# Optimization experiments

Hardware: AMD Instinct MI355X
Metric: run time of the kernel (lower is better)

## Reference

```python
import jax, jax.numpy as jnp
import numpy as np

N_COARSE = 12500
N_FINE = 50000
MIN_BASIS = 16  # (min(L_in, L_out) + 1) ** 2 with L_in = L_out = 3


def setup_inputs() -> dict:
    key = jax.random.key(0)
    ks = jax.random.split(key, 8)
    return {
        "last_inv": jax.random.normal(ks[0], (N_COARSE, 256), dtype=jnp.float32),
        "cur_inv": jax.random.normal(ks[1], (N_FINE, 256), dtype=jnp.float32),
        "last_equ": jax.random.normal(ks[2], (N_COARSE, 16, 256), dtype=jnp.float32),
        "cur_equ": jax.random.normal(ks[3], (N_FINE, 16, 256), dtype=jnp.float32),
        "upsampling": jax.random.randint(ks[4], (N_FINE,), 0, N_COARSE, dtype=jnp.int32),
        # Linear weights stored as [in, out] (torch weight is [out, in]; x @ W.T == x @ W_in_out)
        "W_last_equ": jax.random.normal(ks[5], (256, 256), dtype=jnp.float32) * 0.02,
        "W_cur_equ": jax.random.normal(ks[6], (256, 256), dtype=jnp.float32) * 0.02,
        "W_mlp": jax.random.normal(ks[7], (768, 512), dtype=jnp.float32) * 0.02,
    }


def reference(last_inv, cur_inv, last_equ, cur_equ, upsampling, W_last_equ, W_cur_equ, W_mlp):
    # nearest_upsample: gather coarse rows up to fine resolution
    li = jnp.take(last_inv, upsampling, axis=0)                 # [N_fine, 256]
    le = jnp.take(last_equ, upsampling, axis=0)[:, :MIN_BASIS]  # [N_fine, 16, 256]
    le = jnp.einsum('nbc,cd->nbd', le, W_last_equ)              # fc_last_equ (no bias)
    ce = jnp.einsum('nbc,cd->nbd', cur_equ[:, :MIN_BASIS], W_cur_equ)  # fc_cur_equ
    equ = (ce * le).mean(axis=1)                                # [N_fine, 256]
    com = jnp.concatenate([li, cur_inv, equ], axis=-1)          # [N_fine, 768]
    return com @ W_mlp                                          # LastUnaryBlock: Linear, no bias
```

## Files before the change

### kernel.cpp

```cpp
#include <hip/hip_runtime.h>
#include <hip/hip_bf16.h>

#define N_COARSE 12500
#define N_FINE   50000

typedef __bf16 bf16x8 __attribute__((ext_vector_type(8)));
typedef __bf16 bf16x4 __attribute__((ext_vector_type(4)));
typedef float  f32x4  __attribute__((ext_vector_type(4)));


__device__ __forceinline__ bf16x8 cvt8(f32x4 x, f32x4 y) {
    bf16x8 r;
    r[0] = (__bf16)x[0]; r[1] = (__bf16)x[1]; r[2] = (__bf16)x[2]; r[3] = (__bf16)x[3];
    r[4] = (__bf16)y[0]; r[5] = (__bf16)y[1]; r[6] = (__bf16)y[2]; r[7] = (__bf16)y[3];
    return r;
}

__device__ __forceinline__ void lds_barrier() {
    asm volatile("s_waitcnt lgkmcnt(0)" ::: "memory");
    __builtin_amdgcn_s_barrier();
}

__device__ __forceinline__ void gl_lds16(const float* g, float* l) {
    __builtin_amdgcn_global_load_lds(
        (const __attribute__((address_space(1))) void*)g,
        (__attribute__((address_space(3))) void*)l, 16, 0, 0);
}

__device__ __forceinline__ int swz(int row, int byte) { return byte ^ ((row & 7) << 4); }
__device__ __forceinline__ void st_a(__bf16* lds, int row, int cs, bf16x8 v) {
    *(bf16x8*)((char*)lds + swz(row, row * 512 + cs * 16)) = v;
}
__device__ __forceinline__ bf16x8 ld_a(const __bf16* lds, int row, int ka) {
    return *(const bf16x8*)((const char*)lds + swz(row, row * 512 + ka * 2));
}

template<int NT>
__device__ __forceinline__ void stage_f32(const float* __restrict__ A, long row0,
                                          __bf16* lds, int tid, long maxrow) {
    const int r0 = tid >> 5, cs = tid & 31;
    constexpr int RPI = NT / 32;
    #pragma unroll
    for (int i = 0; i < 64 / RPI; ++i) {
        int row = r0 + i * RPI;
        long gr = row0 + row; if (gr > maxrow) gr = maxrow;
        const float* p = A + gr * 256 + cs * 8;
        f32x4 x = *(const f32x4*)p, y = *(const f32x4*)(p + 4);
        st_a(lds, row, cs, cvt8(x, y));
    }
}

__device__ __forceinline__ void mfma_tile(const __bf16* lds, const bf16x8* __restrict__ packB,
                                          int N, int c0, int ksb,
                                          f32x4 (&acc)[4][4], int lane) {
    const int g = lane >> 4, r15 = lane & 15;
    #pragma unroll
    for (int ks = 0; ks < 8; ++ks) {
        bf16x8 a[4];
        #pragma unroll
        for (int rt = 0; rt < 4; ++rt)
            a[rt] = ld_a(lds, rt * 16 + r15, ks * 32 + g * 8);
        const size_t kb = (size_t)((ksb + ks) * 4 + g) * N;
        #pragma unroll
        for (int ct = 0; ct < 4; ++ct) {
            bf16x8 b = packB[kb + c0 + ct * 16 + r15];
            #pragma unroll
            for (int rt = 0; rt < 4; ++rt)
                acc[rt][ct] = __builtin_amdgcn_mfma_f32_16x16x32_bf16(a[rt], b, acc[rt][ct], 0, 0, 0);
        }
    }
}

__global__ __launch_bounds__(256) void k_prep(
    const float* __restrict__ W_le, const float* __restrict__ W_ce,
    const float* __restrict__ W_mlp, const float* __restrict__ last_inv,
    __bf16* __restrict__ packLE, __bf16* __restrict__ packCE,
    __bf16* __restrict__ packM, __bf16* __restrict__ li_bf)
{
    const int b = blockIdx.x, tid = threadIdx.x;
    if (b < 256) {
        int idx = b * 256 + tid, k = idx >> 8, n = idx & 255;
        packLE[(((size_t)(k >> 3) << 8) + n) * 8 + (k & 7)] = (__bf16)W_le[idx];
    } else if (b < 512) {
        int idx = (b - 256) * 256 + tid, k = idx >> 8, n = idx & 255;
        packCE[(((size_t)(k >> 3) << 8) + n) * 8 + (k & 7)] = (__bf16)W_ce[idx];
    } else if (b < 2048) {
        int idx = (b - 512) * 256 + tid, k = idx >> 9, n = idx & 511;
        packM[(((size_t)(k >> 3) << 9) + n) * 8 + (k & 7)] = (__bf16)W_mlp[idx];
    } else {
        int i = (b - 2048) * 256 + tid;
        f32x4 v = ((const f32x4*)last_inv)[i];
        bf16x4 o;
        o[0] = (__bf16)v[0]; o[1] = (__bf16)v[1]; o[2] = (__bf16)v[2]; o[3] = (__bf16)v[3];
        ((bf16x4*)li_bf)[i] = o;
    }
}

__global__ __launch_bounds__(256) void k_coarse_equ(
    const float* __restrict__ last_equ, const bf16x8* __restrict__ packW,
    __bf16* __restrict__ LEp)
{
    __shared__ __attribute__((aligned(16))) __bf16 As[64 * 256];
    const int tid = threadIdx.x, lane = tid & 63, wid = tid >> 6;
    for (int t = blockIdx.x; t < N_COARSE * 16 / 64; t += gridDim.x) {
        stage_f32<256>(last_equ, (long)t * 64, As, tid, (long)N_COARSE * 16 - 1);
        lds_barrier();
        f32x4 acc[4][4] = {};
        mfma_tile(As, packW, 256, wid * 64, 0, acc, lane);
        #pragma unroll
        for (int rt = 0; rt < 4; ++rt) {
            int coarse = t * 4 + rt;
            #pragma unroll
            for (int ct = 0; ct < 4; ++ct) {
                int cg = wid * 4 + ct;
                bf16x4 v;
                v[0] = (__bf16)acc[rt][ct][0]; v[1] = (__bf16)acc[rt][ct][1];
                v[2] = (__bf16)acc[rt][ct][2]; v[3] = (__bf16)acc[rt][ct][3];
                *(bf16x4*)(LEp + ((size_t)(coarse * 16 + cg) * 64 + lane) * 4) = v;
            }
        }
        lds_barrier();
    }
}

__global__ __launch_bounds__(256) void k_fine_equ(
    const float* __restrict__ cur_equ, const bf16x8* __restrict__ packW,
    const __bf16* __restrict__ LEp, const int* __restrict__ up,
    __bf16* __restrict__ equ)
{
    __shared__ __attribute__((aligned(16))) float Af[2][32 * 256];
    const int tid = threadIdx.x, lane = tid & 63, wid = tid >> 6;
    const int g = lane >> 4, r15 = lane & 15;
    const int NT = N_FINE / 2;
    const int per = (NT + gridDim.x - 1) / gridDim.x;
    const int tb = blockIdx.x * per;
    const int te = min(tb + per, NT);
    if (tb >= te) return;

    const int lhalf = (lane & 1) << 2;

    {
        const float* rb = cur_equ + (size_t)tb * 32 * 256;
        #pragma unroll
        for (int i = 0; i < 8; ++i) {
            int row = wid * 8 + i;
            gl_lds16(rb + (size_t)row * 256 + ((((lane >> 1) ^ (row & 7)) << 3) + lhalf),
                     &Af[tb & 1][row * 256]);
        }
    }

    for (int t = tb; t < te; ++t) {
        asm volatile("s_waitcnt vmcnt(0)" ::: "memory");
        __builtin_amdgcn_s_barrier();

        if (t + 1 < te) {
            const float* rb = cur_equ + (size_t)(t + 1) * 32 * 256;
            #pragma unroll
            for (int i = 0; i < 8; ++i) {
                int row = wid * 8 + i;
                gl_lds16(rb + (size_t)row * 256 + ((((lane >> 1) ^ (row & 7)) << 3) + lhalf),
                         &Af[(t + 1) & 1][row * 256]);
            }
        }

        const float* B = Af[t & 1];
        f32x4 acc[2][4] = {};
        #pragma unroll
        for (int ks = 0; ks < 8; ++ks) {
            bf16x8 a[2];
            #pragma unroll
            for (int rt = 0; rt < 2; ++rt) {
                int r = rt * 16 + r15;
                const float* p = B + r * 256 + (((4 * ks + g) ^ (r & 7)) << 3);
                a[rt] = cvt8(*(const f32x4*)p, *(const f32x4*)(p + 4));
            }
            const size_t kb = (size_t)(ks * 4 + g) * 256;
            #pragma unroll
            for (int ct = 0; ct < 4; ++ct) {
                bf16x8 b = packW[kb + wid * 64 + ct * 16 + r15];
                #pragma unroll
                for (int rt = 0; rt < 2; ++rt)
                    acc[rt][ct] = __builtin_amdgcn_mfma_f32_16x16x32_bf16(a[rt], b, acc[rt][ct], 0, 0, 0);
            }
        }

        const int n0 = t * 2;
        const int cu0 = up[n0], cu1 = up[n0 + 1];
        bf16x4 le[2][4];
        #pragma unroll
        for (int ct = 0; ct < 4; ++ct) {
            le[0][ct] = *(const bf16x4*)(LEp + ((size_t)(cu0 * 16 + wid * 4 + ct) * 64 + lane) * 4);
            le[1][ct] = *(const bf16x4*)(LEp + ((size_t)(cu1 * 16 + wid * 4 + ct) * 64 + lane) * 4);
        }
        #pragma unroll
        for (int rt = 0; rt < 2; ++rt) {
            #pragma unroll
            for (int ct = 0; ct < 4; ++ct) {
                float s = acc[rt][ct][0] * (float)le[rt][ct][0]
                        + acc[rt][ct][1] * (float)le[rt][ct][1]
                        + acc[rt][ct][2] * (float)le[rt][ct][2]
                        + acc[rt][ct][3] * (float)le[rt][ct][3];
                s += __shfl_xor(s, 16, 64);
                s += __shfl_xor(s, 32, 64);
                if (lane < 16)
                    equ[(size_t)(n0 + rt) * 256 + wid * 64 + ct * 16 + lane] =
                        (__bf16)(s * 0.0625f);
            }
        }
    }
}

__global__ __launch_bounds__(512) void k_out(
    const __bf16* __restrict__ li_bf, const float* __restrict__ cur_inv,
    const __bf16* __restrict__ equ, const bf16x8* __restrict__ packW,
    const int* __restrict__ up, float* __restrict__ out)
{
    __shared__ __attribute__((aligned(16))) __bf16 As[64 * 256];
    const int tid = threadIdx.x, lane = tid & 63, wid = tid >> 6;
    const int row0 = blockIdx.x * 64;
    const int c0 = wid * 64;
    const int r0 = tid >> 5, cs = tid & 31;
    f32x4 acc[4][4] = {};

    #pragma unroll
    for (int i = 0; i < 4; ++i) {
        int row = r0 + i * 16;
        int gr = row0 + row; if (gr > N_FINE - 1) gr = N_FINE - 1;
        st_a(As, row, cs, *(const bf16x8*)(li_bf + (size_t)up[gr] * 256 + cs * 8));
    }
    lds_barrier();
    mfma_tile(As, packW, 512, c0, 0, acc, lane);
    lds_barrier();

    stage_f32<512>(cur_inv, row0, As, tid, N_FINE - 1);
    lds_barrier();
    mfma_tile(As, packW, 512, c0, 8, acc, lane);
    lds_barrier();

    #pragma unroll
    for (int i = 0; i < 4; ++i) {
        int row = r0 + i * 16;
        int gr = row0 + row; if (gr > N_FINE - 1) gr = N_FINE - 1;
        st_a(As, row, cs, *(const bf16x8*)(equ + (size_t)gr * 256 + cs * 8));
    }
    lds_barrier();
    mfma_tile(As, packW, 512, c0, 16, acc, lane);

    const int g = lane >> 4, r15 = lane & 15;
    #pragma unroll
    for (int rt = 0; rt < 4; ++rt)
        #pragma unroll
        for (int j = 0; j < 4; ++j) {
            int r = row0 + rt * 16 + g * 4 + j;
            if (r < N_FINE)
                #pragma unroll
                for (int ct = 0; ct < 4; ++ct)
                    out[(size_t)r * 512 + c0 + ct * 16 + r15] = acc[rt][ct][j];
        }
}

extern "C" void kernel_launch(void* const* d_in, const int* in_sizes, int n_in,
                              void* d_out, int out_size, void* d_ws, size_t ws_size,
                              hipStream_t stream) {
    const float* last_inv = (const float*)d_in[0];
    const float* cur_inv  = (const float*)d_in[1];
    const float* last_equ = (const float*)d_in[2];
    const float* cur_equ  = (const float*)d_in[3];
    const int*   up       = (const int*)d_in[4];
    const float* W_le     = (const float*)d_in[5];
    const float* W_ce     = (const float*)d_in[6];
    const float* W_mlp    = (const float*)d_in[7];
    float* out = (float*)d_out;

    char* w = (char*)d_ws;
    __bf16* LEp    = (__bf16*)w;  w += (size_t)N_COARSE * 16 * 256 * 2;
    __bf16* equ    = (__bf16*)w;  w += (size_t)N_FINE * 256 * 2;
    __bf16* li_bf  = (__bf16*)w;  w += (size_t)N_COARSE * 256 * 2;
    __bf16* packLE = (__bf16*)w;  w += (size_t)256 * 256 * 2;
    __bf16* packCE = (__bf16*)w;  w += (size_t)256 * 256 * 2;
    __bf16* packM  = (__bf16*)w;  w += (size_t)768 * 512 * 2;

    k_prep<<<2048 + 3125, 256, 0, stream>>>(
        W_le, W_ce, W_mlp, last_inv, packLE, packCE, packM, li_bf);

    k_coarse_equ<<<1280, 256, 0, stream>>>(
        last_equ, (const bf16x8*)packLE, LEp);

    k_fine_equ<<<512, 256, 0, stream>>>(
        cur_equ, (const bf16x8*)packCE, LEp, up, equ);

    k_out<<<(N_FINE + 63) / 64, 512, 0, stream>>>(
        li_bf, cur_inv, equ, (const bf16x8*)packM, up, out);
}
```

Before: 516.4 us.

## Double-buffer coarse equ kernel with async global-to-LDS loads

```diff
diff --git a/kernel.cpp b/kernel.cpp
--- a/kernel.cpp
+++ b/kernel.cpp
@@ -100,16 +100,65 @@
     const float* __restrict__ last_equ, const bf16x8* __restrict__ packW,
     __bf16* __restrict__ LEp)
 {
-    __shared__ __attribute__((aligned(16))) __bf16 As[64 * 256];
+    __shared__ __attribute__((aligned(16))) float Af[2][32 * 256];
     const int tid = threadIdx.x, lane = tid & 63, wid = tid >> 6;
-    for (int t = blockIdx.x; t < N_COARSE * 16 / 64; t += gridDim.x) {
-        stage_f32<256>(last_equ, (long)t * 64, As, tid, (long)N_COARSE * 16 - 1);
-        lds_barrier();
-        f32x4 acc[4][4] = {};
-        mfma_tile(As, packW, 256, wid * 64, 0, acc, lane);
-        #pragma unroll
-        for (int rt = 0; rt < 4; ++rt) {
-            int coarse = t * 4 + rt;
+    const int g = lane >> 4, r15 = lane & 15;
+    const int NT = N_COARSE * 16 / 32;
+    const int per = (NT + gridDim.x - 1) / gridDim.x;
+    const int tb = blockIdx.x * per;
+    const int te = min(tb + per, NT);
+    if (tb >= te) return;
+
+    const int lhalf = (lane & 1) << 2;
+
+    {
+        const float* rb = last_equ + (size_t)tb * 32 * 256;
+        #pragma unroll
+        for (int i = 0; i < 8; ++i) {
+            int row = wid * 8 + i;
+            gl_lds16(rb + (size_t)row * 256 + ((((lane >> 1) ^ (row & 7)) << 3) + lhalf),
+                     &Af[tb & 1][row * 256]);
+        }
+    }
+
+    for (int t = tb; t < te; ++t) {
+        asm volatile("s_waitcnt vmcnt(0)" ::: "memory");
+        __builtin_amdgcn_s_barrier();
+
+        if (t + 1 < te) {
+            const float* rb = last_equ + (size_t)(t + 1) * 32 * 256;
+            #pragma unroll
+            for (int i = 0; i < 8; ++i) {
+                int row = wid * 8 + i;
+                gl_lds16(rb + (size_t)row * 256 + ((((lane >> 1) ^ (row & 7)) << 3) + lhalf),
+                         &Af[(t + 1) & 1][row * 256]);
+            }
+        }
+
+        const float* B = Af[t & 1];
+        f32x4 acc[2][4] = {};
+        #pragma unroll
+        for (int ks = 0; ks < 8; ++ks) {
+            bf16x8 a[2];
+            #pragma unroll
+            for (int rt = 0; rt < 2; ++rt) {
+                int r = rt * 16 + r15;
+                const float* p = B + r * 256 + (((4 * ks + g) ^ (r & 7)) << 3);
+                a[rt] = cvt8(*(const f32x4*)p, *(const f32x4*)(p + 4));
+            }
+            const size_t kb = (size_t)(ks * 4 + g) * 256;
+            #pragma unroll
+            for (int ct = 0; ct < 4; ++ct) {
+                bf16x8 b = packW[kb + wid * 64 + ct * 16 + r15];
+                #pragma unroll
+                for (int rt = 0; rt < 2; ++rt)
+                    acc[rt][ct] = __builtin_amdgcn_mfma_f32_16x16x32_bf16(a[rt], b, acc[rt][ct], 0, 0, 0);
+            }
+        }
+
+        #pragma unroll
+        for (int rt = 0; rt < 2; ++rt) {
+            int coarse = t * 2 + rt;
             #pragma unroll
             for (int ct = 0; ct < 4; ++ct) {
                 int cg = wid * 4 + ct;
@@ -119,7 +168,6 @@
                 *(bf16x4*)(LEp + ((size_t)(coarse * 16 + cg) * 64 + lane) * 4) = v;
             }
         }
-        lds_barrier();
     }
 }
 
@@ -283,7 +331,7 @@
     k_prep<<<2048 + 3125, 256, 0, stream>>>(
         W_le, W_ce, W_mlp, last_inv, packLE, packCE, packM, li_bf);
 
-    k_coarse_equ<<<1280, 256, 0, stream>>>(
+    k_coarse_equ<<<512, 256, 0, stream>>>(
         last_equ, (const bf16x8*)packLE, LEp);
 
     k_fine_equ<<<512, 256, 0, stream>>>(
```

Result: faster. 483.4 us (-6.4%).
